# Optimization experiments

Measured on AMD Instinct MI355X. Metric: run time of the kernel, lower is better.

The kernel has to match this reference:

```python
import jax, jax.numpy as jnp
import numpy as np

EPS = 1e-12  # F.normalize default eps
TEMPERATURE = 1.0


def _l2_normalize(x):
    n = jnp.sqrt(jnp.sum(x * x, axis=-1, keepdims=True))
    return x / jnp.maximum(n, EPS)


def setup_inputs() -> dict:
    key = jax.random.key(0)
    k1, k2 = jax.random.split(key)
    B, C, H, W = 16, 256, 128, 256
    K = 19
    features = jax.random.normal(k1, (B, C, H, W), dtype=jnp.float32)
    prototypes = jax.random.normal(k2, (K, C), dtype=jnp.float32)
    distance_scale = jnp.ones((1,), dtype=jnp.float32)
    return {"features": features, "prototypes": prototypes,
            "distance_scale": distance_scale}


def reference(features, prototypes, distance_scale):
    B, C, H, W = features.shape
    K = prototypes.shape[0]
    # [B,C,H,W] -> [B*H*W, C]
    x = features.transpose(0, 2, 3, 1).reshape(-1, C)
    xn = _l2_normalize(x)            # [N, C]
    pn = _l2_normalize(prototypes)   # [K, C]
    # pairwise Euclidean distance via the stable quadratic expansion
    # ||a-b||^2 = ||a||^2 + ||b||^2 - 2 a.b  (norms ~1 after normalization)
    xx = jnp.sum(xn * xn, axis=-1)   # [N]
    pp = jnp.sum(pn * pn, axis=-1)   # [K]
    d2 = xx[:, None] + pp[None, :] - 2.0 * jnp.einsum('nc,kc->nk', xn, pn)
    dist = jnp.sqrt(jnp.maximum(d2, 0.0))  # [N, K]
    dist = jnp.abs(distance_scale) * dist
    logits = -dist.reshape(B, H, W, K).transpose(0, 3, 1, 2)  # [B,K,H,W]
    return logits / TEMPERATURE
```

## Files before the change

### kernel.cpp

```cpp
#include <hip/hip_runtime.h>


namespace {
constexpr int kC   = 256;
constexpr int kK   = 19;
constexpr int kKP  = 20;
constexpr int kHW  = 128 * 256;
constexpr int kBlock = 256;
constexpr int kPixPerThread = 4;
}

__global__ __launch_bounds__(kBlock, 2)
void isomax_dist_kernel(const float* __restrict__ feat,
                        const float* __restrict__ proto,
                        const float* __restrict__ dscale,
                        float* __restrict__ out)
{
    __shared__ float pn_s[kC * kKP];
    __shared__ float pp_s[kK];

    const int tid  = threadIdx.x;
    const int lane = tid & 63;
    const int wv   = tid >> 6;

    for (int k = wv; k < kK; k += 4) {
        float v[4];
        float ss = 0.f;
        #pragma unroll
        for (int j = 0; j < 4; ++j) {
            v[j] = proto[k * kC + j * 64 + lane];
            ss = fmaf(v[j], v[j], ss);
        }
        #pragma unroll
        for (int m = 1; m < 64; m <<= 1)
            ss += __shfl_xor(ss, m, 64);
        const float nrm = sqrtf(ss);
        const float inv = 1.0f / fmaxf(nrm, 1e-12f);
        #pragma unroll
        for (int j = 0; j < 4; ++j)
            pn_s[(j * 64 + lane) * kKP + k] = v[j] * inv;
        if (lane == 0) pp_s[k] = ss * inv * inv;
    }
    __syncthreads();

    const int gpix = (blockIdx.x * kBlock + tid) * kPixPerThread;
    const int b    = gpix >> 15;
    const int hw   = gpix & (kHW - 1);
    const float* fp = feat + (size_t)b * kC * kHW + hw;

    float xx[4] = {0.f, 0.f, 0.f, 0.f};
    float4 dot[kK];
    #pragma unroll
    for (int k = 0; k < kK; ++k) dot[k] = make_float4(0.f, 0.f, 0.f, 0.f);

    for (int cc = 0; cc < kC; cc += 4) {
        float4 v[4];
        #pragma unroll
        for (int u = 0; u < 4; ++u)
            v[u] = *(const float4*)(fp + (size_t)(cc + u) * kHW);
        #pragma unroll
        for (int u = 0; u < 4; ++u) {
            const int c = cc + u;
            float4 P[5];
            const float4* row = (const float4*)(pn_s + c * kKP);
            #pragma unroll
            for (int q = 0; q < 5; ++q) P[q] = row[q];
            const float* p = (const float*)P;
            xx[0] = fmaf(v[u].x, v[u].x, xx[0]);
            xx[1] = fmaf(v[u].y, v[u].y, xx[1]);
            xx[2] = fmaf(v[u].z, v[u].z, xx[2]);
            xx[3] = fmaf(v[u].w, v[u].w, xx[3]);
            #pragma unroll
            for (int k = 0; k < kK; ++k) {
                dot[k].x = fmaf(p[k], v[u].x, dot[k].x);
                dot[k].y = fmaf(p[k], v[u].y, dot[k].y);
                dot[k].z = fmaf(p[k], v[u].z, dot[k].z);
                dot[k].w = fmaf(p[k], v[u].w, dot[k].w);
            }
        }
    }

    float inv[4], xnsq[4];
    #pragma unroll
    for (int j = 0; j < 4; ++j) {
        const float nrm = sqrtf(xx[j]);
        inv[j]  = 1.0f / fmaxf(nrm, 1e-12f);
        xnsq[j] = xx[j] * inv[j] * inv[j];
    }
    const float sc = fabsf(dscale[0]);

    float* op = out + (size_t)b * kK * kHW + hw;
    #pragma unroll
    for (int k = 0; k < kK; ++k) {
        const float ppk = pp_s[k];
        float4 o;
        o.x = -sc * sqrtf(fmaxf(xnsq[0] + ppk - 2.0f * dot[k].x * inv[0], 0.f));
        o.y = -sc * sqrtf(fmaxf(xnsq[1] + ppk - 2.0f * dot[k].y * inv[1], 0.f));
        o.z = -sc * sqrtf(fmaxf(xnsq[2] + ppk - 2.0f * dot[k].z * inv[2], 0.f));
        o.w = -sc * sqrtf(fmaxf(xnsq[3] + ppk - 2.0f * dot[k].w * inv[3], 0.f));
        *(float4*)(op + (size_t)k * kHW) = o;
    }
}

extern "C" void kernel_launch(void* const* d_in, const int* in_sizes, int n_in,
                              void* d_out, int out_size, void* d_ws, size_t ws_size,
                              hipStream_t stream) {
    const float* feat   = (const float*)d_in[0];
    const float* proto  = (const float*)d_in[1];
    const float* dscale = (const float*)d_in[2];
    float* out = (float*)d_out;

    const int npix    = in_sizes[0] / kC;
    const int threads = npix / kPixPerThread;
    const dim3 grid(threads / kBlock);
    isomax_dist_kernel<<<grid, kBlock, 0, stream>>>(feat, proto, dscale, out);
}
```

Baseline: 693.9 us.

## Precompute normalized prototypes in separate kernel, use nontemporal loads/stores, unroll 8

Moves prototype normalization into a one-block kernel that writes to workspace, so the main kernel reads prototype rows from global memory (uniform, cached loads) instead of per-block shared memory setup and a barrier. The channel loop now issues 8 nontemporal float4 feature loads per iteration, and outputs are written with nontemporal stores to reduce cache pollution on streaming data. This removes the per-block prologue and sync but adds a second launch and relies on cache hits for the prototype reads, with higher register pressure from the deeper unroll.

```diff
diff --git a/kernel.cpp b/kernel.cpp
--- a/kernel.cpp
+++ b/kernel.cpp
@@ -1,28 +1,25 @@
 #include <hip/hip_runtime.h>
 
 
+typedef float f4 __attribute__((ext_vector_type(4)));
+
 namespace {
-constexpr int kC   = 256;
-constexpr int kK   = 19;
-constexpr int kKP  = 20;
-constexpr int kHW  = 128 * 256;
+constexpr int kC     = 256;
+constexpr int kK     = 19;
+constexpr int kKP    = 20;
+constexpr int kHW    = 128 * 256;
 constexpr int kBlock = 256;
-constexpr int kPixPerThread = 4;
+constexpr int kPix   = 4;
+constexpr int kUnroll= 8;
 }
 
-__global__ __launch_bounds__(kBlock, 2)
-void isomax_dist_kernel(const float* __restrict__ feat,
-                        const float* __restrict__ proto,
-                        const float* __restrict__ dscale,
-                        float* __restrict__ out)
+__global__ void proto_norm_kernel(const float* __restrict__ proto,
+                                  float* __restrict__ pn,
+                                  float* __restrict__ pp)
 {
-    __shared__ float pn_s[kC * kKP];
-    __shared__ float pp_s[kK];
-
     const int tid  = threadIdx.x;
     const int lane = tid & 63;
     const int wv   = tid >> 6;
-
     for (int k = wv; k < kK; k += 4) {
         float v[4];
         float ss = 0.f;
@@ -34,37 +31,46 @@
         #pragma unroll
         for (int m = 1; m < 64; m <<= 1)
             ss += __shfl_xor(ss, m, 64);
-        const float nrm = sqrtf(ss);
-        const float inv = 1.0f / fmaxf(nrm, 1e-12f);
+        const float inv = 1.0f / fmaxf(sqrtf(ss), 1e-12f);
         #pragma unroll
         for (int j = 0; j < 4; ++j)
-            pn_s[(j * 64 + lane) * kKP + k] = v[j] * inv;
-        if (lane == 0) pp_s[k] = ss * inv * inv;
+            pn[(j * 64 + lane) * kKP + k] = v[j] * inv;
+        if (lane == 0) pp[k] = ss * inv * inv;
     }
-    __syncthreads();
+    if (tid < kC) pn[tid * kKP + kK] = 0.f;
+}
 
-    const int gpix = (blockIdx.x * kBlock + tid) * kPixPerThread;
+__global__ __launch_bounds__(kBlock, 2)
+void isomax_main(const float* __restrict__ feat,
+                 const float* __restrict__ pn,
+                 const float* __restrict__ pp,
+                 const float* __restrict__ dscale,
+                 float* __restrict__ out)
+{
+    const int tid  = threadIdx.x;
+    const int gpix = (blockIdx.x * kBlock + tid) * kPix;
     const int b    = gpix >> 15;
     const int hw   = gpix & (kHW - 1);
     const float* fp = feat + (size_t)b * kC * kHW + hw;
 
     float xx[4] = {0.f, 0.f, 0.f, 0.f};
-    float4 dot[kK];
+    f4 dot[kK];
     #pragma unroll
-    for (int k = 0; k < kK; ++k) dot[k] = make_float4(0.f, 0.f, 0.f, 0.f);
+    for (int k = 0; k < kK; ++k) dot[k] = (f4)(0.f);
 
-    for (int cc = 0; cc < kC; cc += 4) {
-        float4 v[4];
+    for (int cc = 0; cc < kC; cc += kUnroll) {
+        f4 v[kUnroll];
         #pragma unroll
-        for (int u = 0; u < 4; ++u)
-            v[u] = *(const float4*)(fp + (size_t)(cc + u) * kHW);
+        for (int u = 0; u < kUnroll; ++u)
+            v[u] = __builtin_nontemporal_load(
+                       (const f4*)(fp + (size_t)(cc + u) * kHW));
         #pragma unroll
-        for (int u = 0; u < 4; ++u) {
+        for (int u = 0; u < kUnroll; ++u) {
             const int c = cc + u;
-            float4 P[5];
-            const float4* row = (const float4*)(pn_s + c * kKP);
+            const f4* __restrict__ prow = (const f4*)(pn + (size_t)c * kKP);
+            f4 P[5];
             #pragma unroll
-            for (int q = 0; q < 5; ++q) P[q] = row[q];
+            for (int q = 0; q < 5; ++q) P[q] = prow[q];
             const float* p = (const float*)P;
             xx[0] = fmaf(v[u].x, v[u].x, xx[0]);
             xx[1] = fmaf(v[u].y, v[u].y, xx[1]);
@@ -83,8 +89,7 @@
     float inv[4], xnsq[4];
     #pragma unroll
     for (int j = 0; j < 4; ++j) {
-        const float nrm = sqrtf(xx[j]);
-        inv[j]  = 1.0f / fmaxf(nrm, 1e-12f);
+        inv[j]  = 1.0f / fmaxf(sqrtf(xx[j]), 1e-12f);
         xnsq[j] = xx[j] * inv[j] * inv[j];
     }
     const float sc = fabsf(dscale[0]);
@@ -92,13 +97,13 @@
     float* op = out + (size_t)b * kK * kHW + hw;
     #pragma unroll
     for (int k = 0; k < kK; ++k) {
-        const float ppk = pp_s[k];
-        float4 o;
+        const float ppk = pp[k];
+        f4 o;
         o.x = -sc * sqrtf(fmaxf(xnsq[0] + ppk - 2.0f * dot[k].x * inv[0], 0.f));
         o.y = -sc * sqrtf(fmaxf(xnsq[1] + ppk - 2.0f * dot[k].y * inv[1], 0.f));
         o.z = -sc * sqrtf(fmaxf(xnsq[2] + ppk - 2.0f * dot[k].z * inv[2], 0.f));
         o.w = -sc * sqrtf(fmaxf(xnsq[3] + ppk - 2.0f * dot[k].w * inv[3], 0.f));
-        *(float4*)(op + (size_t)k * kHW) = o;
+        __builtin_nontemporal_store(o, (f4*)(op + (size_t)k * kHW));
     }
 }
 
@@ -110,8 +115,13 @@
     const float* dscale = (const float*)d_in[2];
     float* out = (float*)d_out;
 
+    float* pn = (float*)d_ws;
+    float* pp = pn + kC * kKP;
+
+    proto_norm_kernel<<<dim3(1), dim3(256), 0, stream>>>(proto, pn, pp);
+
     const int npix    = in_sizes[0] / kC;
-    const int threads = npix / kPixPerThread;
-    const dim3 grid(threads / kBlock);
-    isomax_dist_kernel<<<grid, kBlock, 0, stream>>>(feat, proto, dscale, out);
+    const int threads = npix / kPix;
+    isomax_main<<<dim3(threads / kBlock), dim3(kBlock), 0, stream>>>(
+        feat, pn, pp, dscale, out);
 }
```

New measurement: 695.3 us. Within noise of the previous version (+0.2%).
